# Performance work log

Measured on AMD Instinct MI355X. Metric: run time of the kernel, lower is better.

Reference implementation:

```python
import jax, jax.numpy as jnp
import numpy as np

N_VERTS = 2562


def _uniform(key, shape, bound):
    return jax.random.uniform(key, shape, jnp.float32, -bound, bound)


def vert_align(feat, pos):
    # feat: [B,C,H,W]; pos: [B,N,3], xy in [-1,1] -> bilinear sample -> [B,N,C]
    B, C, H, W = feat.shape
    ft = jnp.transpose(feat, (0, 2, 3, 1))  # [B,H,W,C]
    x = (jnp.clip(pos[..., 0], -1.0, 1.0) + 1.0) * 0.5 * (W - 1)
    y = (jnp.clip(pos[..., 1], -1.0, 1.0) + 1.0) * 0.5 * (H - 1)
    x0 = jnp.floor(x)
    y0 = jnp.floor(y)
    x0i = x0.astype(jnp.int32)
    y0i = y0.astype(jnp.int32)
    x1i = jnp.minimum(x0i + 1, W - 1)
    y1i = jnp.minimum(y0i + 1, H - 1)
    wx = (x - x0)[..., None]
    wy = (y - y0)[..., None]
    b = jnp.arange(B)[:, None]
    f00 = ft[b, y0i, x0i]
    f01 = ft[b, y0i, x1i]
    f10 = ft[b, y1i, x0i]
    f11 = ft[b, y1i, x1i]
    return (f00 * (1 - wx) * (1 - wy) + f01 * wx * (1 - wy)
            + f10 * (1 - wx) * wy + f11 * wx * wy)


def graph_conv(x, adj, w0, w1):
    # relu(x @ w0 + adj @ (x @ w1))
    return jax.nn.relu(x @ w0 + jnp.einsum('bij,bjc->bic', adj, x @ w1))


def setup_inputs() -> dict:
    key = jax.random.key(0)
    ks = jax.random.split(key, 20)
    B, N = 8, N_VERTS
    inp = {
        'conv2_3': jax.random.normal(ks[0], (B, 256, 56, 56), jnp.float32),
        'conv3_4': jax.random.normal(ks[1], (B, 512, 28, 28), jnp.float32),
        'conv4_6': jax.random.normal(ks[2], (B, 1024, 14, 14), jnp.float32),
        'conv5_3': jax.random.normal(ks[3], (B, 2048, 7, 7), jnp.float32),
        # scaled so row sums are O(1), like a normalized dense adjacency
        'vertex_adjacency': jax.random.uniform(ks[4], (B, N, N), jnp.float32) * (2.0 / N),
        'vertex_positions': jax.random.uniform(ks[5], (B, N, 3), jnp.float32) * 2.0 - 1.0,
        'vertex_features': jax.random.normal(ks[6], (B, N, 128), jnp.float32),
    }
    # learned parameters (torch default / GraphConv uniform init)
    inp['w_lin0'] = _uniform(ks[7], (3840, 128), 1.0 / np.sqrt(3840))
    inp['b_lin0'] = _uniform(ks[8], (128,), 1.0 / np.sqrt(3840))
    inp['gc0_w0'] = _uniform(ks[9], (259, 131), 1.0 / np.sqrt(259))
    inp['gc0_w1'] = _uniform(ks[10], (259, 131), 1.0 / np.sqrt(259))
    inp['gc1_w0'] = _uniform(ks[11], (131, 128), 1.0 / np.sqrt(131))
    inp['gc1_w1'] = _uniform(ks[12], (131, 128), 1.0 / np.sqrt(131))
    inp['gc2_w0'] = _uniform(ks[13], (131, 128), 1.0 / np.sqrt(131))
    inp['gc2_w1'] = _uniform(ks[14], (131, 128), 1.0 / np.sqrt(131))
    inp['w_lin1'] = _uniform(ks[15], (128, 3), 1.0 / np.sqrt(128))
    inp['b_lin1'] = _uniform(ks[16], (3,), 1.0 / np.sqrt(128))
    return inp


def reference(conv2_3, conv3_4, conv4_6, conv5_3, vertex_adjacency,
              vertex_positions, vertex_features,
              w_lin0, b_lin0, gc0_w0, gc0_w1, gc1_w0, gc1_w1,
              gc2_w0, gc2_w1, w_lin1, b_lin1):
    verts = jnp.concatenate(
        [vert_align(f, vertex_positions)
         for f in (conv2_3, conv3_4, conv4_6, conv5_3)], axis=2)  # [B,N,3840]
    projected = verts @ w_lin0 + b_lin0                             # [B,N,128]
    vf = jnp.concatenate([vertex_features, vertex_positions, projected], axis=2)  # 259
    h = graph_conv(vf, vertex_adjacency, gc0_w0, gc0_w1)            # [B,N,131]
    h = jnp.concatenate([vertex_positions, h], axis=2)              # 134? no: 3+131=134 -- see note
    h = graph_conv(h[:, :, :131] if h.shape[2] != 131 else h, vertex_adjacency, gc1_w0, gc1_w1)
    h = jnp.concatenate([vertex_positions, h], axis=2)              # 131
    new_features = graph_conv(h, vertex_adjacency, gc2_w0, gc2_w1)  # [B,N,128]
    new_positions = vertex_positions + jnp.tanh(new_features @ w_lin1 + b_lin1)
    return new_positions, new_features
```

## Files before the change

### kernel.cpp

```cpp
#include <hip/hip_runtime.h>
#include <hip/hip_bf16.h>

typedef __attribute__((ext_vector_type(8))) short bf16x8;
typedef __attribute__((ext_vector_type(4))) float f32x4;
typedef __attribute__((ext_vector_type(2))) float f32x2;
typedef long long i64;

static __device__ __forceinline__ float bf2f(unsigned short u){
  return __uint_as_float(((unsigned)u) << 16);
}
static __device__ __forceinline__ float bflo(unsigned v){ return __uint_as_float(v << 16); }
static __device__ __forceinline__ float bfhi(unsigned v){ return __uint_as_float(v & 0xffff0000u); }
static __device__ __forceinline__ unsigned short f2bf(float f){
  unsigned u = __float_as_uint(f);
  u += 0x7FFFu + ((u >> 16) & 1u);
  return (unsigned short)(u >> 16);
}
static __device__ __forceinline__ unsigned f2e4m3(float x){
  unsigned b = __float_as_uint(x);
  unsigned s = (b >> 31) << 7;
  b &= 0x7fffffffu;
  if (b >= 0x43e80000u) return s | 0x7eu;
  if (b < 0x3c800000u)
    return s | (unsigned)rintf(__uint_as_float(b) * 512.f);
  unsigned b2 = b + 0x7ffffu + ((b >> 20) & 1u);
  return s | (((b2 >> 23) - 120u) << 3) | ((b2 >> 20) & 7u);
}
static __device__ __forceinline__ void gload_lds16(const void* g, void* l){
  __builtin_amdgcn_global_load_lds((const __attribute__((address_space(1))) unsigned int*)g,
                                   (__attribute__((address_space(3))) unsigned int*)l, 16, 0, 0);
}

#define MFMA16(acc, a, b) (acc) = __builtin_amdgcn_mfma_f32_16x16x32_bf16((a),(b),(acc),0,0,0)
#define MFMA8(acc, a, b)  (acc) = __builtin_amdgcn_mfma_f32_16x16x32_fp8_fp8((a),(b),(acc),0,0,0)

#define NB    8
#define NVRT  2562
#define MP    2624
#define NRB2  82
#define NRB16 164
#define NKT8  21
#define KOCT  336
#define YO    ((size_t)KOCT*128*8)

#define FT_B0 0ul
#define FT_B1 6422528ul
#define FT_B2 9633792ul
#define FT_B3 11239424ul
#define FT_TOT 12042240ul

#define G_B0 0ul
#define G_B1 3211264ul
#define G_B2 4014080ul
#define G_B3 4214784ul
#define G_TOT 4264960ul

__global__ void k_transpose_all(const float* __restrict__ c0, const float* __restrict__ c1,
                                const float* __restrict__ c2, const float* __restrict__ c3,
                                unsigned short* __restrict__ ftT)
{
  __shared__ float tile[32][33];
  int bx = blockIdx.x, b = blockIdx.y;
  int m, local;
  if (bx < 784)      { m = 0; local = bx; }
  else if (bx < 1184){ m = 1; local = bx - 784; }
  else if (bx < 1408){ m = 2; local = bx - 1184; }
  else               { m = 3; local = bx - 1408; }
  int HW  = (m==0)?3136:(m==1)?784:(m==2)?196:49;
  int C   = 256 << m;
  int nbx = (m==0)?98:(m==1)?25:(m==2)?7:2;
  size_t fb = (m==0)?FT_B0:(m==1)?FT_B1:(m==2)?FT_B2:FT_B3;
  const float* src = (m==0)?c0:(m==1)?c1:(m==2)?c2:c3;

  int hw0 = (local % nbx) * 32, c0i = (local / nbx) * 32;
  int tx = threadIdx.x, ty = threadIdx.y;
  const float* s = src + (size_t)b * C * HW;
#pragma unroll
  for (int i = 0; i < 4; i++){
    int c = c0i + ty + i*8, hw = hw0 + tx;
    tile[ty + i*8][tx] = (c < C && hw < HW) ? s[(size_t)c * HW + hw] : 0.f;
  }
  __syncthreads();
  unsigned short* d = ftT + fb + (size_t)b * HW * C;
#pragma unroll
  for (int i = 0; i < 4; i++){
    int hw = hw0 + ty + i*8, c = c0i + tx;
    if (hw < HW && c < C) d[(size_t)hw * C + c] = f2bf(tile[tx][ty + i*8]);
  }
}

struct PWArgs {
  const float* src[7];
  unsigned short* dst[7];
  int ksrc[7], nsrc[7];
};
__global__ void k_packw_all(PWArgs a)
{
  const int cb[8] = {0,491520,528384,565248,585728,606208,626688,647168};
  int g = blockIdx.x * 256 + threadIdx.x;
#pragma unroll
  for (int s = 0; s < 7; s++){
    if (g >= cb[s] && g < cb[s+1]){
      int li = g - cb[s];
      int k = li >> 7, c = li & 127;
      int ks = a.ksrc[s], ns = a.nsrc[s];
      float v = (k < ks) ? a.src[s][(size_t)k * ns + c] : 0.f;
      a.dst[s][((size_t)(k >> 3) * 128 + c) * 8 + (k & 7)] = f2bf(v);
    }
  }
}

__global__ __launch_bounds__(256) void k_gproj(
    const unsigned short* __restrict__ ftT,
    const unsigned short* __restrict__ wp,
    unsigned short* __restrict__ G)
{
  int bx = blockIdx.x;
  int m, tile;
  if (bx < 784)      { m = 0; tile = bx; }
  else if (bx < 980) { m = 1; tile = bx - 784; }
  else if (bx < 1029){ m = 2; tile = bx - 980; }
  else               { m = 3; tile = bx - 1029; }
  int C    = 256 << m;
  int rows = 8 * ((m==0)?3136:(m==1)?784:(m==2)?196:49);
  size_t fb = (m==0)?FT_B0:(m==1)?FT_B1:(m==2)?FT_B2:FT_B3;
  size_t gb = (m==0)?G_B0:(m==1)?G_B1:(m==2)?G_B2:G_B3;
  int ko8 = ((m==0)?0:(m==1)?256:(m==2)?768:1792) >> 3;

  int t = threadIdx.x, wave = t >> 6, lane = t & 63;
  int rf = wave & 1, ch = wave >> 1;
  int l15 = lane & 15, l4 = lane >> 4;
  int row = tile*32 + rf*16 + l15;
  int arow = (row < rows) ? row : 0;
  const unsigned short* xp = ftT + fb + (size_t)arow * C + l4 * 8;

  f32x4 acc[4];
#pragma unroll
  for (int c = 0; c < 4; c++) acc[c] = (f32x4){0,0,0,0};

  for (int kb = 0; kb < C; kb += 32){
    bf16x8 a = *(const bf16x8*)(xp + kb);
    size_t bo = ((size_t)(ko8 + (kb>>3) + l4) * 128 + ch*64 + l15) * 8;
#pragma unroll
    for (int c = 0; c < 4; c++){
      bf16x8 bb = *(const bf16x8*)(wp + bo + c*128);
      MFMA16(acc[c], a, bb);
    }
  }
#pragma unroll
  for (int c = 0; c < 4; c++){
    int col = ch*64 + c*16 + l15;
#pragma unroll
    for (int r = 0; r < 4; r++){
      int orow = tile*32 + rf*16 + l4*4 + r;
      if (orow < rows) G[gb + (size_t)orow*128 + col] = f2bf(acc[c][r]);
    }
  }
}

__global__ void k_prep2(const float* __restrict__ vfeat, const float* __restrict__ pos,
                        const unsigned short* __restrict__ G,
                        const float* __restrict__ bias,
                        unsigned short* __restrict__ vf,
                        unsigned short* __restrict__ x1,
                        unsigned short* __restrict__ x2)
{
  int b = blockIdx.y;
  int row = blockIdx.x * 4 + (threadIdx.x >> 6);
  int lane = threadIdx.x & 63;
  size_t vfo = ((size_t)b * MP + row) * 288;
  size_t xo  = ((size_t)b * MP + row) * 160;
  if (row < NVRT){
    size_t src = (size_t)b * NVRT + row;
    float px = fminf(fmaxf(pos[src*3 + 0], -1.f), 1.f);
    float py = fminf(fmaxf(pos[src*3 + 1], -1.f), 1.f);
    int c0 = lane * 2;
    float s0 = bias[c0], s1 = bias[c0 + 1];
#pragma unroll
    for (int m = 0; m < 4; m++){
      int W = 56 >> m;
      int HW = W * W;
      size_t gb = (m==0)?G_B0:(m==1)?G_B1:(m==2)?G_B2:G_B3;
      float gx = (px + 1.f) * 0.5f * (float)(W - 1);
      float gy = (py + 1.f) * 0.5f * (float)(W - 1);
      int x0 = (int)floorf(gx), y0 = (int)floorf(gy);
      float wx = gx - (float)x0, wy = gy - (float)y0;
      int x1i = min(x0 + 1, W - 1), y1i = min(y0 + 1, W - 1);
      const unsigned short* g = G + gb + (size_t)b * HW * 128;
      unsigned v00 = *(const unsigned*)(g + ((size_t)(y0 *W + x0 ))*128 + c0);
      unsigned v01 = *(const unsigned*)(g + ((size_t)(y0 *W + x1i))*128 + c0);
      unsigned v10 = *(const unsigned*)(g + ((size_t)(y1i*W + x0 ))*128 + c0);
      unsigned v11 = *(const unsigned*)(g + ((size_t)(y1i*W + x1i))*128 + c0);
      float w00 = (1.f-wx)*(1.f-wy), w01 = wx*(1.f-wy);
      float w10 = (1.f-wx)*wy,       w11 = wx*wy;
      s0 += w00*bflo(v00) + w01*bflo(v01) + w10*bflo(v10) + w11*bflo(v11);
      s1 += w00*bfhi(v00) + w01*bfhi(v01) + w10*bfhi(v10) + w11*bfhi(v11);
    }
    vf[vfo + 131 + c0]     = f2bf(s0);
    vf[vfo + 131 + c0 + 1] = f2bf(s1);
    float2 fv = *(const float2*)(vfeat + src*128 + c0);
    vf[vfo + c0]     = f2bf(fv.x);
    vf[vfo + c0 + 1] = f2bf(fv.y);
    if (lane < 3){
      unsigned short v = f2bf(pos[src*3 + lane]);
      vf[vfo + 128 + lane] = v;
      x1[xo + lane] = v;
      x2[xo + lane] = v;
    }
    if (lane >= 32 && lane < 61) vf[vfo + 259 + (lane - 32)] = 0;
    if (lane < 29){ x1[xo + 131 + lane] = 0; x2[xo + 131 + lane] = 0; }
  } else {
    for (int c = lane; c < 288; c += 64) vf[vfo + c] = 0;
    for (int c = lane; c < 160; c += 64){ x1[xo + c] = 0; x2[xo + c] = 0; }
  }
}

__global__ void k_adjpack8(const float* __restrict__ adj, unsigned char* __restrict__ adjP)
{
  int kt = blockIdx.x, rb = blockIdx.y, b = blockIdx.z;
  int t = threadIdx.x;
  int r = t >> 4, kseg = t & 15;
  int grow = rb*16 + r, gk = kt*128 + kseg*8;
  float v[8];
  if (grow < NVRT && gk + 8 <= NVRT){
    const float4* p = (const float4*)(adj + ((size_t)b*NVRT + grow)*NVRT + gk);
    float4 f0 = p[0], f1 = p[1];
    v[0]=f0.x; v[1]=f0.y; v[2]=f0.z; v[3]=f0.w;
    v[4]=f1.x; v[5]=f1.y; v[6]=f1.z; v[7]=f1.w;
  } else if (grow < NVRT){
    const float* ap = adj + ((size_t)b*NVRT + grow)*NVRT;
#pragma unroll
    for (int e = 0; e < 8; e++){ int k = gk + e; v[e] = (k < NVRT) ? ap[k] : 0.f; }
  } else {
#pragma unroll
    for (int e = 0; e < 8; e++) v[e] = 0.f;
  }
  unsigned long long q = 0;
#pragma unroll
  for (int e = 0; e < 8; e++)
    q |= (unsigned long long)f2e4m3(v[e] * 1024.f) << (8*e);
  unsigned char* tb = adjP + (((size_t)b*NRB16 + rb)*NKT8 + kt) * 2048;
  *(unsigned long long*)(tb + 128*r + 8*(kseg ^ r)) = q;
}

template<int KX>
__global__ __launch_bounds__(256) void k_xw2(
    const unsigned short* __restrict__ x,
    const unsigned short* __restrict__ wp0,
    const unsigned short* __restrict__ wp1,
    float* __restrict__ y0,
    unsigned char* __restrict__ y1p8)
{
  int b = blockIdx.y, rb = blockIdx.x * 32;
  int t = threadIdx.x, wave = t >> 6, lane = t & 63;
  int rf = wave & 1, ch = wave >> 1;
  int l15 = lane & 15, l4 = lane >> 4;
  f32x4 a0[4], a1[4];
#pragma unroll
  for (int c = 0; c < 4; c++){ a0[c] = (f32x4){0,0,0,0}; a1[c] = (f32x4){0,0,0,0}; }
  int row = rb + rf*16 + l15;
  const unsigned short* xp = x + ((size_t)b * MP + row) * KX + l4 * 8;
#pragma unroll
  for (int kb = 0; kb < KX; kb += 32){
    bf16x8 a = *(const bf16x8*)(xp + kb);
    size_t bo = ((size_t)((kb>>3) + l4) * 128 + ch*64 + l15) * 8;
#pragma unroll
    for (int c = 0; c < 4; c++){
      bf16x8 b0 = *(const bf16x8*)(wp0 + bo + c*128);
      MFMA16(a0[c], a, b0);
      bf16x8 b1 = *(const bf16x8*)(wp1 + bo + c*128);
      MFMA16(a1[c], a, b1);
    }
  }
  unsigned char* yb = y1p8 + (size_t)b * YO;
#pragma unroll
  for (int c = 0; c < 4; c++){
    int col = ch*64 + c*16 + l15;
    int orow0 = rb + rf*16 + l4*4;
#pragma unroll
    for (int r = 0; r < 4; r++)
      y0[((size_t)b * MP + orow0 + r) * 128 + col] = a0[c][r];
    unsigned q = f2e4m3(a1[c][0]) | (f2e4m3(a1[c][1]) << 8)
               | (f2e4m3(a1[c][2]) << 16) | (f2e4m3(a1[c][3]) << 24);
    *(unsigned*)(yb + ((size_t)(orow0 >> 3) * 128 + col) * 8 + (orow0 & 7)) = q;
  }
}

template<int EPI>
__global__ __launch_bounds__(256) void k_adj8(
    const unsigned char* __restrict__ adjP,
    const unsigned char* __restrict__ y1p8,
    const float* __restrict__ y0,
    unsigned short* __restrict__ xnext,
    float* __restrict__ outf,
    const float* __restrict__ pos,
    const float* __restrict__ wl1, const float* __restrict__ bl1,
    float* __restrict__ opos)
{
  __shared__ __align__(16) unsigned char abuf[2][2048];
  __shared__ float hbuf[16][128];
  int rb = blockIdx.x, b = blockIdx.y;
  int t = threadIdx.x, w = t >> 6, lane = t & 63;
  int l15 = lane & 15, l4 = lane >> 4;
  const unsigned char* tb = adjP + (((size_t)b*NRB16 + rb)*NKT8) * 2048;
  const unsigned char* yb = y1p8 + (size_t)b * YO;

  f32x4 acc[2];
  acc[0] = (f32x4){0,0,0,0};
  acc[1] = (f32x4){0,0,0,0};

  auto stage = [&](int kt, int bufi){
    if (w < 2)
      gload_lds16(tb + (size_t)kt*2048 + w*1024 + lane*16, &abuf[bufi][w*1024]);
  };

  stage(0, 0);
  __syncthreads();

  for (int kt = 0; kt < NKT8; ++kt){
    int cur = kt & 1;
    if (kt < NKT8-1) stage(kt+1, cur ^ 1);
    const unsigned char* ab = &abuf[cur][0];
#pragma unroll
    for (int sel = 0; sel < 2; sel++){
#pragma unroll
      for (int ks = 0; ks < 2; ks++){
        int koct = sel*8 + ks*4 + l4;
        i64 a = *(const i64*)(ab + 128*l15 + 8*(koct ^ l15));
        const unsigned char* bp = yb + ((size_t)(kt*16 + koct)*128 + w*32 + l15)*8;
        i64 b0 = *(const i64*)(bp);
        i64 b1 = *(const i64*)(bp + 128);
        MFMA8(acc[0], a, b0);
        MFMA8(acc[1], a, b1);
      }
    }
    __syncthreads();
  }

#pragma unroll
  for (int cf = 0; cf < 2; cf++){
    int col = w*32 + cf*16 + l15;
#pragma unroll
    for (int r = 0; r < 4; r++){
      int row16 = l4*4 + r;
      int row = rb*16 + row16;
      float v = 0.f;
      if (row < NVRT)
        v = fmaxf(y0[((size_t)b*MP + row)*128 + col] + acc[cf][r] * 0.0009765625f, 0.f);
      if (EPI == 0){
        if (row < NVRT) xnext[((size_t)b*MP + row)*160 + 3 + col] = f2bf(v);
      } else {
        if (row < NVRT) outf[((size_t)b*NVRT + row)*128 + col] = v;
        hbuf[row16][col] = v;
      }
    }
  }

  if (EPI == 1){
    __syncthreads();
#pragma unroll
    for (int rr = 0; rr < 4; rr++){
      int row16 = w*4 + rr;
      int grow = rb*16 + row16;
      if (grow < NVRT){
        int c0 = lane * 2;
        float v0 = hbuf[row16][c0], v1 = hbuf[row16][c0+1];
        float p[3];
#pragma unroll
        for (int j = 0; j < 3; j++){
          p[j] = v0 * wl1[c0*3 + j] + v1 * wl1[c0*3 + 3 + j];
#pragma unroll
          for (int off = 1; off < 64; off <<= 1)
            p[j] += __shfl_xor(p[j], off);
        }
        if (lane == 0){
          size_t po = ((size_t)b * NVRT + grow) * 3;
#pragma unroll
          for (int j = 0; j < 3; j++)
            opos[po + j] = pos[po + j] + tanhf(p[j] + bl1[j]);
        }
      }
    }
  }
}

extern "C" void kernel_launch(void* const* d_in, const int* in_sizes, int n_in,
                              void* d_out, int out_size, void* d_ws, size_t ws_size,
                              hipStream_t stream)
{
  const float* conv[4] = {(const float*)d_in[0], (const float*)d_in[1],
                          (const float*)d_in[2], (const float*)d_in[3]};
  const float* adj   = (const float*)d_in[4];
  const float* pos   = (const float*)d_in[5];
  const float* vfeat = (const float*)d_in[6];
  const float* wlin0 = (const float*)d_in[7];
  const float* blin0 = (const float*)d_in[8];
  const float* gw[6] = {(const float*)d_in[9],  (const float*)d_in[10],
                        (const float*)d_in[11], (const float*)d_in[12],
                        (const float*)d_in[13], (const float*)d_in[14]};
  const float* wlin1 = (const float*)d_in[15];
  const float* blin1 = (const float*)d_in[16];

  char* ws = (char*)d_ws;
  size_t off = 0;
  auto take = [&](size_t bytes)->char* {
    char* p = ws + off;
    off += (bytes + 255) & ~(size_t)255;
    return p;
  };
  unsigned short* ftT  = (unsigned short*)take(FT_TOT * 2);
  unsigned short* G    = (unsigned short*)take(G_TOT * 2);
  unsigned char*  adjP = (unsigned char*)take((size_t)NB*NRB16*NKT8*2048);
  unsigned short* wl0p = (unsigned short*)take((size_t)3840*128*2);
  unsigned short* w0p0 = (unsigned short*)take((size_t)288*128*2);
  unsigned short* w1p0 = (unsigned short*)take((size_t)288*128*2);
  unsigned short* w0p1 = (unsigned short*)take((size_t)160*128*2);
  unsigned short* w1p1 = (unsigned short*)take((size_t)160*128*2);
  unsigned short* w0p2 = (unsigned short*)take((size_t)160*128*2);
  unsigned short* w1p2 = (unsigned short*)take((size_t)160*128*2);
  unsigned short* vf   = (unsigned short*)take((size_t)NB*MP*288*2);
  unsigned short* x1   = (unsigned short*)take((size_t)NB*MP*160*2);
  unsigned short* x2   = (unsigned short*)take((size_t)NB*MP*160*2);
  float*          y0   = (float*)take((size_t)NB*MP*128*4);
  unsigned char*  y1p8 = (unsigned char*)take((size_t)NB*YO);

  float* out_pos  = (float*)d_out;
  float* out_feat = out_pos + (size_t)NB*NVRT*3;

  hipMemsetAsync(y1p8, 0, (size_t)NB*YO, stream);
  k_transpose_all<<<dim3(1536, NB), dim3(32, 8), 0, stream>>>(conv[0], conv[1], conv[2], conv[3], ftT);
  PWArgs pw;
  pw.src[0]=wlin0; pw.dst[0]=wl0p; pw.ksrc[0]=3840; pw.nsrc[0]=128;
  pw.src[1]=gw[0]; pw.dst[1]=w0p0; pw.ksrc[1]=259;  pw.nsrc[1]=131;
  pw.src[2]=gw[1]; pw.dst[2]=w1p0; pw.ksrc[2]=259;  pw.nsrc[2]=131;
  pw.src[3]=gw[2]; pw.dst[3]=w0p1; pw.ksrc[3]=131;  pw.nsrc[3]=128;
  pw.src[4]=gw[3]; pw.dst[4]=w1p1; pw.ksrc[4]=131;  pw.nsrc[4]=128;
  pw.src[5]=gw[4]; pw.dst[5]=w0p2; pw.ksrc[5]=131;  pw.nsrc[5]=128;
  pw.src[6]=gw[5]; pw.dst[6]=w1p2; pw.ksrc[6]=131;  pw.nsrc[6]=128;
  k_packw_all<<<2528, 256, 0, stream>>>(pw);
  k_gproj<<<1042, 256, 0, stream>>>(ftT, wl0p, G);
  k_prep2<<<dim3(MP/4, NB), 256, 0, stream>>>(vfeat, pos, G, blin0, vf, x1, x2);
  k_adjpack8<<<dim3(NKT8, NRB16, NB), 256, 0, stream>>>(adj, adjP);
  k_xw2<288><<<dim3(NRB2, NB), 256, 0, stream>>>(vf, w0p0, w1p0, y0, y1p8);
  k_adj8<0><<<dim3(NRB16, NB), 256, 0, stream>>>(adjP, y1p8, y0, x1, nullptr, nullptr, nullptr, nullptr, nullptr);
  k_xw2<160><<<dim3(NRB2, NB), 256, 0, stream>>>(x1, w0p1, w1p1, y0, y1p8);
  k_adj8<0><<<dim3(NRB16, NB), 256, 0, stream>>>(adjP, y1p8, y0, x2, nullptr, nullptr, nullptr, nullptr, nullptr);
  k_xw2<160><<<dim3(NRB2, NB), 256, 0, stream>>>(x2, w0p2, w1p2, y0, y1p8);
  k_adj8<1><<<dim3(NRB16, NB), 256, 0, stream>>>(adjP, y1p8, y0, nullptr, out_feat, pos, wlin1, blin1, out_pos);
  (void)in_sizes; (void)n_in; (void)out_size; (void)ws_size;
}
```

Baseline: 291.7 us.

## Fuse feature transpose into projection GEMM and move x@w0 into adjacency kernel

Drops the separate fp32-to-bf16 transpose pass: the projection kernel now reads the NCHW conv maps directly, converts them to bf16 in registers, and splits K across four waves with an LDS reduction. The x@w0 product is no longer written to an fp32 y0 buffer by the xw kernel. It is recomputed inside each adjacency kernel, which removes that global round trip. The full-buffer memset is replaced by zeroing only the padded tail from the prep kernel. The trade-off is strided, less coalesced conv reads and redundant small GEMM work per adjacency block.

```diff
diff --git a/kernel.cpp b/kernel.cpp
--- a/kernel.cpp
+++ b/kernel.cpp
@@ -6,9 +6,6 @@
 typedef __attribute__((ext_vector_type(2))) float f32x2;
 typedef long long i64;
 
-static __device__ __forceinline__ float bf2f(unsigned short u){
-  return __uint_as_float(((unsigned)u) << 16);
-}
 static __device__ __forceinline__ float bflo(unsigned v){ return __uint_as_float(v << 16); }
 static __device__ __forceinline__ float bfhi(unsigned v){ return __uint_as_float(v & 0xffff0000u); }
 static __device__ __forceinline__ unsigned short f2bf(float f){
@@ -43,51 +40,11 @@
 #define KOCT  336
 #define YO    ((size_t)KOCT*128*8)
 
-#define FT_B0 0ul
-#define FT_B1 6422528ul
-#define FT_B2 9633792ul
-#define FT_B3 11239424ul
-#define FT_TOT 12042240ul
-
 #define G_B0 0ul
 #define G_B1 3211264ul
 #define G_B2 4014080ul
 #define G_B3 4214784ul
 #define G_TOT 4264960ul
-
-__global__ void k_transpose_all(const float* __restrict__ c0, const float* __restrict__ c1,
-                                const float* __restrict__ c2, const float* __restrict__ c3,
-                                unsigned short* __restrict__ ftT)
-{
-  __shared__ float tile[32][33];
-  int bx = blockIdx.x, b = blockIdx.y;
-  int m, local;
-  if (bx < 784)      { m = 0; local = bx; }
-  else if (bx < 1184){ m = 1; local = bx - 784; }
-  else if (bx < 1408){ m = 2; local = bx - 1184; }
-  else               { m = 3; local = bx - 1408; }
-  int HW  = (m==0)?3136:(m==1)?784:(m==2)?196:49;
-  int C   = 256 << m;
-  int nbx = (m==0)?98:(m==1)?25:(m==2)?7:2;
-  size_t fb = (m==0)?FT_B0:(m==1)?FT_B1:(m==2)?FT_B2:FT_B3;
-  const float* src = (m==0)?c0:(m==1)?c1:(m==2)?c2:c3;
-
-  int hw0 = (local % nbx) * 32, c0i = (local / nbx) * 32;
-  int tx = threadIdx.x, ty = threadIdx.y;
-  const float* s = src + (size_t)b * C * HW;
-#pragma unroll
-  for (int i = 0; i < 4; i++){
-    int c = c0i + ty + i*8, hw = hw0 + tx;
-    tile[ty + i*8][tx] = (c < C && hw < HW) ? s[(size_t)c * HW + hw] : 0.f;
-  }
-  __syncthreads();
-  unsigned short* d = ftT + fb + (size_t)b * HW * C;
-#pragma unroll
-  for (int i = 0; i < 4; i++){
-    int hw = hw0 + ty + i*8, c = c0i + tx;
-    if (hw < HW && c < C) d[(size_t)hw * C + c] = f2bf(tile[tx][ty + i*8]);
-  }
-}
 
 struct PWArgs {
   const float* src[7];
@@ -110,51 +67,78 @@
   }
 }
 
-__global__ __launch_bounds__(256) void k_gproj(
-    const unsigned short* __restrict__ ftT,
+__global__ __launch_bounds__(256) void k_gproj2(
+    const float* __restrict__ c0m, const float* __restrict__ c1m,
+    const float* __restrict__ c2m, const float* __restrict__ c3m,
     const unsigned short* __restrict__ wp,
     unsigned short* __restrict__ G)
 {
+  __shared__ f32x4 red[3][1024];
   int bx = blockIdx.x;
-  int m, tile;
-  if (bx < 784)      { m = 0; tile = bx; }
-  else if (bx < 980) { m = 1; tile = bx - 784; }
-  else if (bx < 1029){ m = 2; tile = bx - 980; }
-  else               { m = 3; tile = bx - 1029; }
-  int C    = 256 << m;
-  int rows = 8 * ((m==0)?3136:(m==1)?784:(m==2)?196:49);
-  size_t fb = (m==0)?FT_B0:(m==1)?FT_B1:(m==2)?FT_B2:FT_B3;
-  size_t gb = (m==0)?G_B0:(m==1)?G_B1:(m==2)?G_B2:G_B3;
-  int ko8 = ((m==0)?0:(m==1)?256:(m==2)?768:1792) >> 3;
-
-  int t = threadIdx.x, wave = t >> 6, lane = t & 63;
-  int rf = wave & 1, ch = wave >> 1;
+  int m, b, tile;
+  if (bx < 784)      { m = 0; b = bx / 98;  tile = bx - b*98; }
+  else if (bx < 984) { int l = bx-784;  m = 1; b = l / 25; tile = l - b*25; }
+  else if (bx < 1040){ int l = bx-984;  m = 2; b = l / 7;  tile = l - b*7; }
+  else               { int l = bx-1040; m = 3; b = l >> 1; tile = l & 1; }
+  int C  = 256 << m;
+  int HW = (m==0)?3136:(m==1)?784:(m==2)?196:49;
+  const float* src = ((m==0)?c0m:(m==1)?c1m:(m==2)?c2m:c3m) + (size_t)b * C * HW;
+  size_t gb = ((m==0)?G_B0:(m==1)?G_B1:(m==2)?G_B2:G_B3) + (size_t)b * HW * 128;
+  int ko8 = (m==0)?0:(m==1)?32:(m==2)?96:224;
+
+  int t = threadIdx.x, w = t >> 6, lane = t & 63;
   int l15 = lane & 15, l4 = lane >> 4;
-  int row = tile*32 + rf*16 + l15;
-  int arow = (row < rows) ? row : 0;
-  const unsigned short* xp = ftT + fb + (size_t)arow * C + l4 * 8;
-
-  f32x4 acc[4];
-#pragma unroll
-  for (int c = 0; c < 4; c++) acc[c] = (f32x4){0,0,0,0};
-
-  for (int kb = 0; kb < C; kb += 32){
-    bf16x8 a = *(const bf16x8*)(xp + kb);
-    size_t bo = ((size_t)(ko8 + (kb>>3) + l4) * 128 + ch*64 + l15) * 8;
-#pragma unroll
-    for (int c = 0; c < 4; c++){
-      bf16x8 bb = *(const bf16x8*)(wp + bo + c*128);
-      MFMA16(acc[c], a, bb);
-    }
-  }
-#pragma unroll
-  for (int c = 0; c < 4; c++){
-    int col = ch*64 + c*16 + l15;
-#pragma unroll
-    for (int r = 0; r < 4; r++){
-      int orow = tile*32 + rf*16 + l4*4 + r;
-      if (orow < rows) G[gb + (size_t)orow*128 + col] = f2bf(acc[c][r]);
-    }
+  int hw0 = tile * 32;
+  int ar0 = min(hw0 + l15, HW - 1);
+  int ar1 = min(hw0 + 16 + l15, HW - 1);
+
+  f32x4 acc[2][8];
+#pragma unroll
+  for (int i = 0; i < 2; i++)
+#pragma unroll
+    for (int j = 0; j < 8; j++) acc[i][j] = (f32x4){0,0,0,0};
+
+  int kq = C >> 2;
+  int kbeg = w * kq, klim = kbeg + kq;
+  for (int kb = kbeg; kb < klim; kb += 32){
+    bf16x8 a0, a1;
+#pragma unroll
+    for (int j = 0; j < 8; j++){
+      int cc = kb + l4*8 + j;
+      a0[j] = (short)f2bf(src[(size_t)cc * HW + ar0]);
+      a1[j] = (short)f2bf(src[(size_t)cc * HW + ar1]);
+    }
+    size_t bo = ((size_t)(ko8 + (kb>>3) + l4) * 128 + l15) * 8;
+#pragma unroll
+    for (int cf = 0; cf < 8; cf++){
+      bf16x8 bb = *(const bf16x8*)(wp + bo + cf*128);
+      MFMA16(acc[0][cf], a0, bb);
+      MFMA16(acc[1][cf], a1, bb);
+    }
+  }
+
+  if (w){
+#pragma unroll
+    for (int rf = 0; rf < 2; rf++)
+#pragma unroll
+      for (int cf = 0; cf < 8; cf++)
+        red[w-1][(rf*8+cf)*64 + lane] = acc[rf][cf];
+  }
+  __syncthreads();
+  if (!w){
+#pragma unroll
+    for (int rf = 0; rf < 2; rf++)
+#pragma unroll
+      for (int cf = 0; cf < 8; cf++){
+        int i = (rf*8+cf)*64 + lane;
+        f32x4 s = acc[rf][cf] + red[0][i] + red[1][i] + red[2][i];
+        int col = cf*16 + l15;
+#pragma unroll
+        for (int r = 0; r < 4; r++){
+          int hw = hw0 + rf*16 + l4*4 + r;
+          if (hw < HW) G[gb + (size_t)hw*128 + col] = f2bf(s[r]);
+        }
+      }
   }
 }
 
@@ -163,9 +147,15 @@
                         const float* __restrict__ bias,
                         unsigned short* __restrict__ vf,
                         unsigned short* __restrict__ x1,
-                        unsigned short* __restrict__ x2)
+                        unsigned short* __restrict__ x2,
+                        unsigned char* __restrict__ y1p8)
 {
   int b = blockIdx.y;
+  if (blockIdx.x == 0){
+    unsigned long long* z = (unsigned long long*)(y1p8 + (size_t)b*YO + (size_t)328*128*8);
+    int i = threadIdx.x;
+    z[i*4+0] = 0; z[i*4+1] = 0; z[i*4+2] = 0; z[i*4+3] = 0;
+  }
   int row = blockIdx.x * 4 + (threadIdx.x >> 6);
   int lane = threadIdx.x & 63;
   size_t vfo = ((size_t)b * MP + row) * 288;
@@ -244,20 +234,18 @@
 }
 
 template<int KX>
-__global__ __launch_bounds__(256) void k_xw2(
+__global__ __launch_bounds__(256) void k_y1(
     const unsigned short* __restrict__ x,
-    const unsigned short* __restrict__ wp0,
     const unsigned short* __restrict__ wp1,
-    float* __restrict__ y0,
     unsigned char* __restrict__ y1p8)
 {
   int b = blockIdx.y, rb = blockIdx.x * 32;
   int t = threadIdx.x, wave = t >> 6, lane = t & 63;
   int rf = wave & 1, ch = wave >> 1;
   int l15 = lane & 15, l4 = lane >> 4;
-  f32x4 a0[4], a1[4];
-#pragma unroll
-  for (int c = 0; c < 4; c++){ a0[c] = (f32x4){0,0,0,0}; a1[c] = (f32x4){0,0,0,0}; }
+  f32x4 a1[4];
+#pragma unroll
+  for (int c = 0; c < 4; c++) a1[c] = (f32x4){0,0,0,0};
   int row = rb + rf*16 + l15;
   const unsigned short* xp = x + ((size_t)b * MP + row) * KX + l4 * 8;
 #pragma unroll
@@ -266,8 +254,6 @@
     size_t bo = ((size_t)((kb>>3) + l4) * 128 + ch*64 + l15) * 8;
 #pragma unroll
     for (int c = 0; c < 4; c++){
-      bf16x8 b0 = *(const bf16x8*)(wp0 + bo + c*128);
-      MFMA16(a0[c], a, b0);
       bf16x8 b1 = *(const bf16x8*)(wp1 + bo + c*128);
       MFMA16(a1[c], a, b1);
     }
@@ -277,20 +263,18 @@
   for (int c = 0; c < 4; c++){
     int col = ch*64 + c*16 + l15;
     int orow0 = rb + rf*16 + l4*4;
-#pragma unroll
-    for (int r = 0; r < 4; r++)
-      y0[((size_t)b * MP + orow0 + r) * 128 + col] = a0[c][r];
     unsigned q = f2e4m3(a1[c][0]) | (f2e4m3(a1[c][1]) << 8)
                | (f2e4m3(a1[c][2]) << 16) | (f2e4m3(a1[c][3]) << 24);
     *(unsigned*)(yb + ((size_t)(orow0 >> 3) * 128 + col) * 8 + (orow0 & 7)) = q;
   }
 }
 
-template<int EPI>
+template<int EPI, int KX>
 __global__ __launch_bounds__(256) void k_adj8(
     const unsigned char* __restrict__ adjP,
     const unsigned char* __restrict__ y1p8,
-    const float* __restrict__ y0,
+    const unsigned short* __restrict__ x,
+    const unsigned short* __restrict__ wp0,
     unsigned short* __restrict__ xnext,
     float* __restrict__ outf,
     const float* __restrict__ pos,
@@ -305,9 +289,9 @@
   const unsigned char* tb = adjP + (((size_t)b*NRB16 + rb)*NKT8) * 2048;
   const unsigned char* yb = y1p8 + (size_t)b * YO;
 
-  f32x4 acc[2];
-  acc[0] = (f32x4){0,0,0,0};
-  acc[1] = (f32x4){0,0,0,0};
+  f32x4 acc[2], accW[2];
+  acc[0] = (f32x4){0,0,0,0};  acc[1] = (f32x4){0,0,0,0};
+  accW[0] = (f32x4){0,0,0,0}; accW[1] = (f32x4){0,0,0,0};
 
   auto stage = [&](int kt, int bufi){
     if (w < 2)
@@ -315,6 +299,16 @@
   };
 
   stage(0, 0);
+
+  const unsigned short* xr = x + ((size_t)b*MP + rb*16 + l15)*KX + l4*8;
+#pragma unroll
+  for (int kb = 0; kb < KX; kb += 32){
+    bf16x8 ax = *(const bf16x8*)(xr + kb);
+    size_t bo = ((size_t)((kb>>3) + l4)*128 + w*32 + l15)*8;
+    MFMA16(accW[0], ax, *(const bf16x8*)(wp0 + bo));
+    MFMA16(accW[1], ax, *(const bf16x8*)(wp0 + bo + 128));
+  }
+
   __syncthreads();
 
   for (int kt = 0; kt < NKT8; ++kt){
@@ -344,9 +338,7 @@
     for (int r = 0; r < 4; r++){
       int row16 = l4*4 + r;
       int row = rb*16 + row16;
-      float v = 0.f;
-      if (row < NVRT)
-        v = fmaxf(y0[((size_t)b*MP + row)*128 + col] + acc[cf][r] * 0.0009765625f, 0.f);
+      float v = fmaxf(accW[cf][r] + acc[cf][r] * 0.0009765625f, 0.f);
       if (EPI == 0){
         if (row < NVRT) xnext[((size_t)b*MP + row)*160 + 3 + col] = f2bf(v);
       } else {
@@ -408,7 +400,6 @@
     off += (bytes + 255) & ~(size_t)255;
     return p;
   };
-  unsigned short* ftT  = (unsigned short*)take(FT_TOT * 2);
   unsigned short* G    = (unsigned short*)take(G_TOT * 2);
   unsigned char*  adjP = (unsigned char*)take((size_t)NB*NRB16*NKT8*2048);
   unsigned short* wl0p = (unsigned short*)take((size_t)3840*128*2);
@@ -421,14 +412,11 @@
   unsigned short* vf   = (unsigned short*)take((size_t)NB*MP*288*2);
   unsigned short* x1   = (unsigned short*)take((size_t)NB*MP*160*2);
   unsigned short* x2   = (unsigned short*)take((size_t)NB*MP*160*2);
-  float*          y0   = (float*)take((size_t)NB*MP*128*4);
   unsigned char*  y1p8 = (unsigned char*)take((size_t)NB*YO);
 
   float* out_pos  = (float*)d_out;
   float* out_feat = out_pos + (size_t)NB*NVRT*3;
 
-  hipMemsetAsync(y1p8, 0, (size_t)NB*YO, stream);
-  k_transpose_all<<<dim3(1536, NB), dim3(32, 8), 0, stream>>>(conv[0], conv[1], conv[2], conv[3], ftT);
   PWArgs pw;
   pw.src[0]=wlin0; pw.dst[0]=wl0p; pw.ksrc[0]=3840; pw.nsrc[0]=128;
   pw.src[1]=gw[0]; pw.dst[1]=w0p0; pw.ksrc[1]=259;  pw.nsrc[1]=131;
@@ -438,14 +426,14 @@
   pw.src[5]=gw[4]; pw.dst[5]=w0p2; pw.ksrc[5]=131;  pw.nsrc[5]=128;
   pw.src[6]=gw[5]; pw.dst[6]=w1p2; pw.ksrc[6]=131;  pw.nsrc[6]=128;
   k_packw_all<<<2528, 256, 0, stream>>>(pw);
-  k_gproj<<<1042, 256, 0, stream>>>(ftT, wl0p, G);
-  k_prep2<<<dim3(MP/4, NB), 256, 0, stream>>>(vfeat, pos, G, blin0, vf, x1, x2);
+  k_gproj2<<<1056, 256, 0, stream>>>(conv[0], conv[1], conv[2], conv[3], wl0p, G);
+  k_prep2<<<dim3(MP/4, NB), 256, 0, stream>>>(vfeat, pos, G, blin0, vf, x1, x2, y1p8);
   k_adjpack8<<<dim3(NKT8, NRB16, NB), 256, 0, stream>>>(adj, adjP);
-  k_xw2<288><<<dim3(NRB2, NB), 256, 0, stream>>>(vf, w0p0, w1p0, y0, y1p8);
-  k_adj8<0><<<dim3(NRB16, NB), 256, 0, stream>>>(adjP, y1p8, y0, x1, nullptr, nullptr, nullptr, nullptr, nullptr);
-  k_xw2<160><<<dim3(NRB2, NB), 256, 0, stream>>>(x1, w0p1, w1p1, y0, y1p8);
-  k_adj8<0><<<dim3(NRB16, NB), 256, 0, stream>>>(adjP, y1p8, y0, x2, nullptr, nullptr, nullptr, nullptr, nullptr);
-  k_xw2<160><<<dim3(NRB2, NB), 256, 0, stream>>>(x2, w0p2, w1p2, y0, y1p8);
-  k_adj8<1><<<dim3(NRB16, NB), 256, 0, stream>>>(adjP, y1p8, y0, nullptr, out_feat, pos, wlin1, blin1, out_pos);
+  k_y1<288><<<dim3(NRB2, NB), 256, 0, stream>>>(vf, w1p0, y1p8);
+  k_adj8<0,288><<<dim3(NRB16, NB), 256, 0, stream>>>(adjP, y1p8, vf, w0p0, x1, nullptr, nullptr, nullptr, nullptr, nullptr);
+  k_y1<160><<<dim3(NRB2, NB), 256, 0, stream>>>(x1, w1p1, y1p8);
+  k_adj8<0,160><<<dim3(NRB16, NB), 256, 0, stream>>>(adjP, y1p8, x1, w0p1, x2, nullptr, nullptr, nullptr, nullptr, nullptr);
+  k_y1<160><<<dim3(NRB2, NB), 256, 0, stream>>>(x2, w1p2, y1p8);
+  k_adj8<1,160><<<dim3(NRB16, NB), 256, 0, stream>>>(adjP, y1p8, x2, w0p2, nullptr, out_feat, pos, wlin1, blin1, out_pos);
   (void)in_sizes; (void)n_in; (void)out_size; (void)ws_size;
 }
```

Measured after the change: 270.6 us. -7.3%, faster.
